# Kernel tuning notes

Measured on AMD Instinct MI355X. Metric: run time of the kernel, lower is better.

Reference implementation:

```python
import jax, jax.numpy as jnp
import numpy as np

B = 64        # graphs per batch
N = 1024      # nodes per graph
DEG = 16      # avg degree
E = B * N * DEG
F_IN = 10
H = 128
NC = 10
K1, K2, K3 = 205, 41, 9   # ceil(0.2 * prev_nodes_per_graph)


def _lin(key, fan_in, shape):
    return jax.random.normal(key, shape, jnp.float32) * (1.0 / np.sqrt(fan_in))


def setup_inputs() -> dict:
    key = jax.random.key(0)
    ks = jax.random.split(key, 32)
    x = jax.random.normal(ks[0], (B * N, F_IN), jnp.float32)
    # random intra-graph edges (source_to_target)
    src_l = jax.random.randint(ks[1], (B, N * DEG), 0, N)
    dst_l = jax.random.randint(ks[2], (B, N * DEG), 0, N)
    off = (jnp.arange(B) * N)[:, None]
    edge_index = jnp.stack([(src_l + off).reshape(-1), (dst_l + off).reshape(-1)]).astype(jnp.int32)
    inp = dict(x=x, edge_index=edge_index)
    inp["W1"] = _lin(ks[3], F_IN, (F_IN, H)); inp["b1"] = jnp.zeros((H,), jnp.float32)
    inp["W2"] = _lin(ks[4], H, (H, H));       inp["b2"] = jnp.zeros((H,), jnp.float32)
    inp["W3"] = _lin(ks[5], H, (H, H));       inp["b3"] = jnp.zeros((H,), jnp.float32)
    inp["Ws1"] = _lin(ks[6], H, (H, 1)); inp["bs1"] = jnp.zeros((1,), jnp.float32)
    inp["Ws2"] = _lin(ks[7], H, (H, 1)); inp["bs2"] = jnp.zeros((1,), jnp.float32)
    inp["Ws3"] = _lin(ks[8], H, (H, 1)); inp["bs3"] = jnp.zeros((1,), jnp.float32)
    inp["Wl1"] = _lin(ks[9], 2 * H, (2 * H, H));    inp["bl1"] = jnp.zeros((H,), jnp.float32)
    inp["Wl2"] = _lin(ks[10], H, (H, H // 2));      inp["bl2"] = jnp.zeros((H // 2,), jnp.float32)
    inp["Wl3"] = _lin(ks[11], H // 2, (H // 2, NC)); inp["bl3"] = jnp.zeros((NC,), jnp.float32)
    return inp


def gcn(x, W, b, src, dst, emask, n):
    """PyG GCNConv: symmetric norm with self-loops; masked edges contribute 0."""
    h = x @ W                                   # [n, out]
    w = emask.astype(h.dtype)                   # edge weights (0 for filtered edges)
    deg = jax.ops.segment_sum(w, dst, num_segments=n) + 1.0   # +1 self-loop
    dis = jax.lax.rsqrt(deg)                    # deg^{-1/2}
    norm = dis[src] * dis[dst] * w              # [E]
    out = jax.ops.segment_sum(h[src] * norm[:, None], dst, num_segments=n)
    out = out + h * (dis * dis)[:, None]        # self-loop message
    return out + b


def sagpool(x, src, dst, emask, Ws, bs, cur, k):
    """SAGPool: GCN score -> per-graph top-k -> gather + tanh gate -> filter_adj."""
    n = B * cur
    score = gcn(x, Ws, bs, src, dst, emask, n)[:, 0]          # [n]
    _, idx = jax.lax.top_k(score.reshape(B, cur), k)          # [B, k]
    perm = (idx + (jnp.arange(B) * cur)[:, None]).reshape(-1) # global node ids
    x = x[perm] * jnp.tanh(score[perm])[:, None]
    # filter_adj: remap node ids, drop edges with an unselected endpoint
    new_id = jnp.full((n,), -1, jnp.int32).at[perm].set(jnp.arange(B * k, dtype=jnp.int32))
    nsrc, ndst = new_id[src], new_id[dst]
    emask = emask & (nsrc >= 0) & (ndst >= 0)
    nsrc = jnp.where(emask, nsrc, 0)
    ndst = jnp.where(emask, ndst, 0)
    return x, nsrc, ndst, emask


def readout(x, k):
    xb = x.reshape(B, k, -1)
    return jnp.concatenate([xb.max(axis=1), xb.mean(axis=1)], axis=1)   # [B, 2H]


def reference(x, edge_index, W1, b1, W2, b2, W3, b3,
              Ws1, bs1, Ws2, bs2, Ws3, bs3,
              Wl1, bl1, Wl2, bl2, Wl3, bl3):
    src, dst = edge_index[0], edge_index[1]
    emask = jnp.ones((E,), bool)

    h = jax.nn.relu(gcn(x, W1, b1, src, dst, emask, B * N))
    h, src, dst, emask = sagpool(h, src, dst, emask, Ws1, bs1, N, K1)
    x1 = readout(h, K1)

    h = jax.nn.relu(gcn(h, W2, b2, src, dst, emask, B * K1))
    h, src, dst, emask = sagpool(h, src, dst, emask, Ws2, bs2, K1, K2)
    x2 = readout(h, K2)

    h = jax.nn.relu(gcn(h, W3, b3, src, dst, emask, B * K2))
    h, src, dst, emask = sagpool(h, src, dst, emask, Ws3, bs3, K2, K3)
    x3 = readout(h, K3)

    z = x1 + x2 + x3                             # [B, 2H]
    z = jax.nn.relu(z @ Wl1 + bl1)               # dropout is eval-mode identity
    z = jax.nn.relu(z @ Wl2 + bl2)
    return jax.nn.log_softmax(z @ Wl3 + bl3, axis=-1)
```

## Files before the change

### kernel.cpp

```cpp
#include <hip/hip_runtime.h>
#include <math.h>

#define NB 64
#define N0 1024
#define NEDGE 1048576
#define EPG 16384
#define FIN 10
#define NCLS 10
#define KP1 205
#define KP2 41
#define KP3 9

static inline int ceil_div(int a, int b) { return (a + b - 1) / b; }

__device__ __forceinline__ int block_scan_incl(int v, int* wtot, int lane, int wid) {
    __syncthreads();
    int x = v;
    #pragma unroll
    for (int s = 1; s < 64; s <<= 1) { int tv = __shfl_up(x, s); if (lane >= s) x += tv; }
    if (lane == 63) wtot[wid] = x;
    __syncthreads();
    if (wid == 0) {
        int w = (lane < 16) ? wtot[lane] : 0;
        #pragma unroll
        for (int s = 1; s < 16; s <<= 1) { int tv = __shfl_up(w, s); if (lane >= s) w += tv; }
        if (lane < 16) wtot[lane] = w;
    }
    __syncthreads();
    return x + ((wid > 0) ? wtot[wid - 1] : 0);
}

__device__ __forceinline__ unsigned fkey(float f) {
    unsigned b = __float_as_uint(f);
    return (f >= 0.f) ? (b | 0x80000000u) : ~b;
}

__global__ __launch_bounds__(1024) void build_csr1_k(const int* __restrict__ ei,
                                                     float* __restrict__ disg,
                                                     int* __restrict__ offg,
                                                     int* __restrict__ cntg,
                                                     int2* __restrict__ csr2) {
    __shared__ int cnt[N0];
    __shared__ int cur[N0];
    __shared__ float disl[N0];
    __shared__ int wtot[16];
    int b = blockIdx.x, t = threadIdx.x;
    int lane = t & 63, wid = t >> 6;
    cnt[t] = 0;
    __syncthreads();
    const int ebase = b * EPG;
    const int nbase = b * N0;
    #pragma unroll
    for (int u = 0; u < EPG / 1024; ++u) {
        int d = ei[NEDGE + ebase + u * 1024 + t] - nbase;
        atomicAdd(&cnt[d], 1);
    }
    __syncthreads();
    int v = cnt[t];
    int inc = block_scan_incl(v, wtot, lane, wid);
    int excl = inc - v;
    cur[t] = excl;
    float di = rsqrtf((float)v + 1.0f);
    disl[t] = di;
    offg[nbase + t] = ebase + excl;
    cntg[nbase + t] = v;
    disg[nbase + t] = di;
    __syncthreads();
    #pragma unroll
    for (int u = 0; u < EPG / 1024; ++u) {
        int j = ebase + u * 1024 + t;
        int s = ei[j], d = ei[NEDGE + j] - nbase;
        int pos = atomicAdd(&cur[d], 1);
        int2 o; o.x = s; o.y = __float_as_int(disl[s - nbase]);
        csr2[ebase + pos] = o;
    }
}

__global__ __launch_bounds__(256) void agg10_k(const float* __restrict__ x,
                                               const int2* __restrict__ csr2,
                                               const int* __restrict__ off,
                                               const int* __restrict__ cnt,
                                               const float* __restrict__ dis,
                                               float* __restrict__ y) {
    __shared__ float xl[N0 * 11];
    int b = blockIdx.x >> 2, chunk = blockIdx.x & 3;
    const float* xg = x + (size_t)b * (N0 * FIN);
    for (int u = threadIdx.x; u < N0 * FIN; u += 256) {
        int r = u / FIN, c = u - r * FIN;
        xl[r * 11 + c] = xg[u];
    }
    __syncthreads();
    int li = chunk * 256 + threadIdx.x;
    int i  = b * N0 + li;
    int s0 = off[i], m = cnt[i];
    int base = b * N0;
    float acc[FIN];
    #pragma unroll
    for (int f = 0; f < FIN; ++f) acc[f] = 0.f;
    int j = 0;
    for (; j + 2 <= m; j += 2) {
        int2 e0 = csr2[s0 + j], e1 = csr2[s0 + j + 1];
        int sl0 = (e0.x - base) * 11, sl1 = (e1.x - base) * 11;
        float w0 = __int_as_float(e0.y), w1 = __int_as_float(e1.y);
        #pragma unroll
        for (int f = 0; f < FIN; ++f) acc[f] += xl[sl0 + f] * w0 + xl[sl1 + f] * w1;
    }
    if (j < m) {
        int2 e0 = csr2[s0 + j];
        int sl0 = (e0.x - base) * 11;
        float w0 = __int_as_float(e0.y);
        #pragma unroll
        for (int f = 0; f < FIN; ++f) acc[f] += xl[sl0 + f] * w0;
    }
    float di = dis[i], d2 = di * di;
    #pragma unroll
    for (int f = 0; f < FIN; ++f)
        y[(size_t)i * FIN + f] = di * acc[f] + d2 * xl[li * 11 + f];
}

__global__ void gemm_fin_fused_k(const float* __restrict__ y, const float* __restrict__ W,
                                 const float* __restrict__ bb, const float* __restrict__ Wsc,
                                 const float* __restrict__ dis,
                                 float* __restrict__ hout, float* __restrict__ hs,
                                 float* __restrict__ hsd, int n) {
    __shared__ float Ws[FIN * 128];
    __shared__ float Sc[128];
    for (int u = threadIdx.x; u < FIN * 128; u += 256) Ws[u] = W[u];
    if (threadIdx.x < 128) Sc[threadIdx.x] = Wsc[threadIdx.x];
    __syncthreads();
    int t = blockIdx.x * 256 + threadIdx.x;
    int i = t >> 6, lane = threadIdx.x & 63;
    if (i >= n) return;
    float a = (lane < FIN) ? y[(size_t)i * FIN + lane] : 0.f;
    const float2* W2 = (const float2*)Ws;
    float ax = bb[lane * 2], ay = bb[lane * 2 + 1];
    #pragma unroll
    for (int k = 0; k < FIN; ++k) {
        float ak = __shfl(a, k);
        float2 w = W2[k * 64 + lane];
        ax += ak * w.x; ay += ak * w.y;
    }
    ax = fmaxf(ax, 0.f); ay = fmaxf(ay, 0.f);
    float2 o; o.x = ax; o.y = ay;
    ((float2*)hout)[(size_t)i * 64 + lane] = o;
    float part = ax * Sc[lane * 2] + ay * Sc[lane * 2 + 1];
    #pragma unroll
    for (int sh = 32; sh >= 1; sh >>= 1) part += __shfl_xor(part, sh);
    if (lane == 0) { hs[i] = part; hsd[i] = part * dis[i]; }
}

__global__ __launch_bounds__(1024) void s1_topk_build2_k(
    const float* __restrict__ hout, const float* __restrict__ hs,
    const float* __restrict__ hsd, const int* __restrict__ ei,
    int2* __restrict__ csr,
    const int* __restrict__ off1, const int* __restrict__ cnt1,
    const float* __restrict__ dis1, const float* __restrict__ bs1,
    float* __restrict__ hA, float* __restrict__ z, int* __restrict__ newid1,
    int* __restrict__ off2, int* __restrict__ cnt2g, float* __restrict__ dis2g,
    int* __restrict__ dst2, int* __restrict__ etot2) {
    __shared__ float hl[1024];
    __shared__ unsigned u[1024];
    __shared__ int wtot[16];
    __shared__ unsigned tinfo[2];
    __shared__ int   n1l[1024];
    __shared__ int   seln[KP1];
    __shared__ float gatel[KP1];
    __shared__ float zm[1024];
    __shared__ float zs[1024];
    __shared__ int   c2[KP1];
    __shared__ int   cur2[KP1];
    __shared__ float d2l[KP1];
    int b = blockIdx.x, t = threadIdx.x;
    int lane = t & 63, wid = t >> 6;
    const int nbase = b * N0, ebase = b * EPG;

    hl[t] = hsd[nbase + t];
    __syncthreads();
    float sc;
    {
        int s0 = off1[nbase + t], e0 = s0 + cnt1[nbase + t];
        float acc = 0.f;
        int j = s0;
        for (; j + 4 <= e0; j += 4) {
            int a0 = csr[j].x, a1 = csr[j+1].x, a2 = csr[j+2].x, a3 = csr[j+3].x;
            acc += hl[a0 - nbase] + hl[a1 - nbase] + hl[a2 - nbase] + hl[a3 - nbase];
        }
        for (; j < e0; ++j) acc += hl[csr[j].x - nbase];
        float di = dis1[nbase + t];
        sc = di * acc + hs[nbase + t] * (di * di) + bs1[0];
    }
    unsigned kb = fkey(sc);
    u[t] = kb;
    __syncthreads();
    if (wid == 0) {
        int remaining = KP1; unsigned prefix = 0;
        for (int bit = 31; bit >= 0; --bit) {
            int c = 0;
            #pragma unroll 4
            for (int i = lane; i < 1024; i += 64)
                c += ((u[i] >> bit) == ((prefix >> bit) | 1u));
            #pragma unroll
            for (int s = 32; s >= 1; s >>= 1) c += __shfl_xor(c, s);
            if (c >= remaining) prefix |= (1u << bit);
            else remaining -= c;
        }
        if (lane == 0) { tinfo[0] = prefix; tinfo[1] = (unsigned)remaining; }
    }
    __syncthreads();
    unsigned T = tinfo[0]; int extra = (int)tinfo[1];
    int gt = (kb > T), eq = (kb == T);
    int eqIncl = block_scan_incl(eq, wtot, lane, wid);
    int sel = gt || (eq && (eqIncl - eq) < extra);
    int selIncl = block_scan_incl(sel, wtot, lane, wid);
    int loc = selIncl - sel;
    if (sel) {
        n1l[t] = loc; seln[loc] = t; gatel[loc] = tanhf(sc);
        newid1[nbase + t] = b * KP1 + loc;
    } else {
        n1l[t] = -1; newid1[nbase + t] = -1;
    }
    __syncthreads();
    {
        int g = t >> 7, f = t & 127;
        float vmax = -INFINITY, vsum = 0.f;
        for (int j = g; j < KP1; j += 8) {
            int src = nbase + seln[j];
            float val = hout[(size_t)src * 128 + f] * gatel[j];
            hA[((size_t)b * KP1 + j) * 128 + f] = val;
            vmax = fmaxf(vmax, val); vsum += val;
        }
        zm[t] = vmax; zs[t] = vsum;
        __syncthreads();
        if (t < 128) {
            float m = zm[t], s2 = zs[t];
            #pragma unroll
            for (int g2 = 1; g2 < 8; ++g2) { m = fmaxf(m, zm[g2 * 128 + t]); s2 += zs[g2 * 128 + t]; }
            z[b * 256 + t] = m;
            z[b * 256 + 128 + t] = s2 / (float)KP1;
        }
    }
    __syncthreads();
    if (t < KP1) c2[t] = 0;
    __syncthreads();
    #pragma unroll
    for (int uu = 0; uu < EPG / 1024; ++uu) {
        int j = ebase + uu * 1024 + t;
        int s = ei[j] - nbase, d = ei[NEDGE + j] - nbase;
        int ls = n1l[s], ld = n1l[d];
        if (ls >= 0 && ld >= 0) atomicAdd(&c2[ld], 1);
    }
    __syncthreads();
    int vv = (t < KP1) ? c2[t] : 0;
    int inc = block_scan_incl(vv, wtot, lane, wid);
    int excl = inc - vv;
    if (t < KP1) {
        cur2[t] = excl;
        float dd = rsqrtf((float)vv + 1.0f);
        d2l[t] = dd;
        off2[b * KP1 + t] = ebase + excl;
        cnt2g[b * KP1 + t] = vv;
        dis2g[b * KP1 + t] = dd;
    }
    if (t == 1023) etot2[b] = inc;
    __syncthreads();
    #pragma unroll
    for (int uu = 0; uu < EPG / 1024; ++uu) {
        int j = ebase + uu * 1024 + t;
        int s = ei[j] - nbase, d = ei[NEDGE + j] - nbase;
        int ls = n1l[s], ld = n1l[d];
        if (ls < 0 || ld < 0) continue;
        int pos = atomicAdd(&cur2[ld], 1);
        int2 o; o.x = b * KP1 + ls; o.y = __float_as_int(d2l[ls]);
        csr[ebase + pos] = o;
        dst2[ebase + pos] = ld;
    }
}

__global__ __launch_bounds__(256) void gemm128_tiled_k(const float* __restrict__ A,
                                                       const float* __restrict__ W,
                                                       float* __restrict__ C, int n) {
    __shared__ float As[64][33];
    __shared__ float Wt[32][64];
    int tx = threadIdx.x & 15, ty = threadIdx.x >> 4;
    int r0 = blockIdx.x * 64;
    int c0 = blockIdx.y * 64;
    float4 acc0 = {0,0,0,0}, acc1 = {0,0,0,0}, acc2 = {0,0,0,0}, acc3 = {0,0,0,0};
    int u = threadIdx.x;
    for (int k0 = 0; k0 < 128; k0 += 32) {
        __syncthreads();
        {
            int rr = u >> 3, cc = (u & 7) * 4;
            #pragma unroll
            for (int h = 0; h < 2; ++h) {
                int r = rr + h * 32;
                float4 v = {0,0,0,0};
                if (r0 + r < n) v = *(const float4*)&A[(size_t)(r0 + r) * 128 + k0 + cc];
                As[r][cc] = v.x; As[r][cc+1] = v.y; As[r][cc+2] = v.z; As[r][cc+3] = v.w;
            }
        }
        {
            int kk = u >> 4, c = (u & 15) * 4;
            #pragma unroll
            for (int h = 0; h < 2; ++h) {
                float4 v = *(const float4*)&W[(size_t)(k0 + kk + h * 16) * 128 + c0 + c];
                *(float4*)&Wt[kk + h * 16][c] = v;
            }
        }
        __syncthreads();
        #pragma unroll
        for (int kk = 0; kk < 32; ++kk) {
            float4 wv = *(const float4*)&Wt[kk][tx * 4];
            float a0 = As[ty * 4 + 0][kk];
            float a1 = As[ty * 4 + 1][kk];
            float a2 = As[ty * 4 + 2][kk];
            float a3 = As[ty * 4 + 3][kk];
            acc0.x += a0 * wv.x; acc0.y += a0 * wv.y; acc0.z += a0 * wv.z; acc0.w += a0 * wv.w;
            acc1.x += a1 * wv.x; acc1.y += a1 * wv.y; acc1.z += a1 * wv.z; acc1.w += a1 * wv.w;
            acc2.x += a2 * wv.x; acc2.y += a2 * wv.y; acc2.z += a2 * wv.z; acc2.w += a2 * wv.w;
            acc3.x += a3 * wv.x; acc3.y += a3 * wv.y; acc3.z += a3 * wv.z; acc3.w += a3 * wv.w;
        }
    }
    int r = r0 + ty * 4;
    if (r + 0 < n) *(float4*)&C[(size_t)(r + 0) * 128 + c0 + tx * 4] = acc0;
    if (r + 1 < n) *(float4*)&C[(size_t)(r + 1) * 128 + c0 + tx * 4] = acc1;
    if (r + 2 < n) *(float4*)&C[(size_t)(r + 2) * 128 + c0 + tx * 4] = acc2;
    if (r + 3 < n) *(float4*)&C[(size_t)(r + 3) * 128 + c0 + tx * 4] = acc3;
}

__global__ void gcn_agg_fused2_k(const float* __restrict__ hW, const int2* __restrict__ csr2,
                                 const int* __restrict__ off, const int* __restrict__ cnt,
                                 const float* __restrict__ dis, const float* __restrict__ bias,
                                 const float* __restrict__ Wsc,
                                 float* __restrict__ hout, float* __restrict__ hs,
                                 float* __restrict__ hsd, int n, int cpx) {
    int wg = ((blockIdx.x & 7) * cpx) + (blockIdx.x >> 3);
    int t = wg * blockDim.x + threadIdx.x;
    int i = t >> 6;
    int lane = threadIdx.x & 63;
    if (i >= n) return;
    const float2* hW2 = (const float2*)hW;
    int s0 = off[i], e0 = s0 + cnt[i];
    float accx = 0.f, accy = 0.f;
    for (int j0 = s0; j0 < e0; j0 += 64) {
        int rem = e0 - j0;
        int m = rem < 64 ? rem : 64;
        int sv = 0; float wv = 0.f;
        if (lane < m) { int2 ec = csr2[j0 + lane]; sv = ec.x; wv = __int_as_float(ec.y); }
        int u = 0;
        for (; u + 4 <= m; u += 4) {
            int a0 = __shfl(sv, u + 0), a1 = __shfl(sv, u + 1);
            int a2 = __shfl(sv, u + 2), a3 = __shfl(sv, u + 3);
            float w0 = __shfl(wv, u + 0), w1 = __shfl(wv, u + 1);
            float w2 = __shfl(wv, u + 2), w3 = __shfl(wv, u + 3);
            float2 v0 = hW2[(size_t)a0 * 64 + lane];
            float2 v1 = hW2[(size_t)a1 * 64 + lane];
            float2 v2 = hW2[(size_t)a2 * 64 + lane];
            float2 v3 = hW2[(size_t)a3 * 64 + lane];
            accx += v0.x * w0 + v1.x * w1 + v2.x * w2 + v3.x * w3;
            accy += v0.y * w0 + v1.y * w1 + v2.y * w2 + v3.y * w3;
        }
        for (; u < m; ++u) {
            int s = __shfl(sv, u);
            float w = __shfl(wv, u);
            float2 v = hW2[(size_t)s * 64 + lane];
            accx += v.x * w; accy += v.y * w;
        }
    }
    float di = dis[i];
    float2 hv = hW2[(size_t)i * 64 + lane];
    float ox = fmaxf(di * accx + hv.x * (di * di) + bias[lane * 2], 0.f);
    float oy = fmaxf(di * accy + hv.y * (di * di) + bias[lane * 2 + 1], 0.f);
    float2 o; o.x = ox; o.y = oy;
    ((float2*)hout)[(size_t)i * 64 + lane] = o;
    float part = ox * Wsc[lane * 2] + oy * Wsc[lane * 2 + 1];
    #pragma unroll
    for (int sh = 32; sh >= 1; sh >>= 1) part += __shfl_xor(part, sh);
    if (lane == 0) { hs[i] = part; hsd[i] = part * di; }
}

__global__ __launch_bounds__(1024) void s2_topk_build3_k(
    const float* __restrict__ hout, const float* __restrict__ hs,
    const float* __restrict__ hsd,
    int2* __restrict__ csr, const int* __restrict__ dst2, const int* __restrict__ etot2,
    const int* __restrict__ off2, const int* __restrict__ cnt2,
    const float* __restrict__ dis2, const float* __restrict__ bs2,
    float* __restrict__ hA, float* __restrict__ z,
    int* __restrict__ off3, int* __restrict__ cnt3g, float* __restrict__ dis3g) {
    __shared__ float hl[256];
    __shared__ unsigned u2[256];
    __shared__ int wtot[16];
    __shared__ unsigned tinfo[2];
    __shared__ int   n2l[KP1];
    __shared__ int   seln[KP2];
    __shared__ float gatel[KP2];
    __shared__ float zm[1024];
    __shared__ float zs[1024];
    __shared__ int   c3[KP2];
    __shared__ int   cur3[KP2];
    __shared__ float d3l[KP2];
    int b = blockIdx.x, t = threadIdx.x;
    int lane = t & 63, wid = t >> 6;
    const int ebase = b * EPG;

    if (t < KP1) hl[t] = hsd[b * KP1 + t];
    __syncthreads();
    float sc = -INFINITY;
    if (t < KP1) {
        int i = b * KP1 + t;
        int s0 = off2[i], e0 = s0 + cnt2[i];
        float acc = 0.f;
        int j = s0;
        for (; j + 4 <= e0; j += 4) {
            int a0 = csr[j].x, a1 = csr[j+1].x, a2 = csr[j+2].x, a3 = csr[j+3].x;
            acc += hl[a0 - b*KP1] + hl[a1 - b*KP1] + hl[a2 - b*KP1] + hl[a3 - b*KP1];
        }
        for (; j < e0; ++j) acc += hl[csr[j].x - b*KP1];
        float di = dis2[i];
        sc = di * acc + hs[i] * (di * di) + bs2[0];
    }
    unsigned kb = fkey(sc);
    if (t < 256) u2[t] = kb;
    __syncthreads();
    if (wid == 0) {
        int remaining = KP2; unsigned prefix = 0;
        for (int bit = 31; bit >= 0; --bit) {
            int c = 0;
            #pragma unroll
            for (int i = lane; i < 256; i += 64)
                c += ((u2[i] >> bit) == ((prefix >> bit) | 1u));
            #pragma unroll
            for (int s = 32; s >= 1; s >>= 1) c += __shfl_xor(c, s);
            if (c >= remaining) prefix |= (1u << bit);
            else remaining -= c;
        }
        if (lane == 0) { tinfo[0] = prefix; tinfo[1] = (unsigned)remaining; }
    }
    __syncthreads();
    unsigned T = tinfo[0]; int extra = (int)tinfo[1];
    int valid = (t < KP1);
    int gt = valid && (kb > T), eq = valid && (kb == T);
    int eqIncl = block_scan_incl(eq, wtot, lane, wid);
    int sel = gt || (eq && (eqIncl - eq) < extra);
    int selIncl = block_scan_incl(sel, wtot, lane, wid);
    int loc = selIncl - sel;
    if (valid) {
        if (sel) { n2l[t] = loc; seln[loc] = t; gatel[loc] = tanhf(sc); }
        else     n2l[t] = -1;
    }
    __syncthreads();
    {
        int g = t >> 7, f = t & 127;
        float vmax = -INFINITY, vsum = 0.f;
        for (int j = g; j < KP2; j += 8) {
            int src = b * KP1 + seln[j];
            float val = hout[(size_t)src * 128 + f] * gatel[j];
            hA[((size_t)b * KP2 + j) * 128 + f] = val;
            vmax = fmaxf(vmax, val); vsum += val;
        }
        zm[t] = vmax; zs[t] = vsum;
        __syncthreads();
        if (t < 128) {
            float m = zm[t], s2 = zs[t];
            #pragma unroll
            for (int g2 = 1; g2 < 8; ++g2) { m = fmaxf(m, zm[g2 * 128 + t]); s2 += zs[g2 * 128 + t]; }
            z[b * 256 + t] += m;
            z[b * 256 + 128 + t] += s2 / (float)KP2;
        }
    }
    __syncthreads();
    int nE2 = etot2[b];
    int es[2], ed[2];
    #pragma unroll
    for (int r = 0; r < 2; ++r) {
        int i = r * 1024 + t;
        if (i < nE2) { es[r] = csr[ebase + i].x - b * KP1; ed[r] = dst2[ebase + i]; }
        else es[r] = -1;
    }
    __syncthreads();
    if (t < KP2) c3[t] = 0;
    __syncthreads();
    int ms[2], md[2];
    #pragma unroll
    for (int r = 0; r < 2; ++r) {
        ms[r] = -1;
        if (es[r] >= 0) {
            int ls = n2l[es[r]], ld = n2l[ed[r]];
            if (ls >= 0 && ld >= 0) { ms[r] = ls; md[r] = ld; atomicAdd(&c3[ld], 1); }
        }
    }
    __syncthreads();
    int vv = (t < KP2) ? c3[t] : 0;
    int inc = block_scan_incl(vv, wtot, lane, wid);
    int excl = inc - vv;
    if (t < KP2) {
        cur3[t] = excl;
        float dd = rsqrtf((float)vv + 1.0f);
        d3l[t] = dd;
        off3[b * KP2 + t] = ebase + excl;
        cnt3g[b * KP2 + t] = vv;
        dis3g[b * KP2 + t] = dd;
    }
    __syncthreads();
    #pragma unroll
    for (int r = 0; r < 2; ++r) {
        if (ms[r] < 0) continue;
        int pos = atomicAdd(&cur3[md[r]], 1);
        int2 o; o.x = b * KP2 + ms[r]; o.y = __float_as_int(d3l[ms[r]]);
        csr[ebase + pos] = o;
    }
}

__global__ __launch_bounds__(128) void s3_topk_mlp_k(
    const float* __restrict__ hout, const float* __restrict__ hs,
    const float* __restrict__ hsd, const int2* __restrict__ csr,
    const int* __restrict__ off3, const int* __restrict__ cnt3,
    const float* __restrict__ dis3, const float* __restrict__ bs3,
    const float* __restrict__ z,
    const float* __restrict__ Wl1, const float* __restrict__ bl1,
    const float* __restrict__ Wl2, const float* __restrict__ bl2,
    const float* __restrict__ Wl3, const float* __restrict__ bl3,
    float* __restrict__ out) {
    __shared__ float hl[KP2];
    __shared__ float v[64];
    __shared__ int   ix[64];
    __shared__ float zm[KP3];
    __shared__ float zr[256], h1[128], h2[64], lg[NCLS], red[2];
    int b = blockIdx.x, t = threadIdx.x;

    if (t < KP2) hl[t] = hsd[b * KP2 + t];
    __syncthreads();
    float sc = -INFINITY;
    if (t < KP2) {
        int i = b * KP2 + t;
        int s0 = off3[i], e0 = s0 + cnt3[i];
        float acc = 0.f;
        for (int j = s0; j < e0; ++j) acc += hl[csr[j].x - b*KP2];
        float di = dis3[i];
        sc = di * acc + hs[i] * (di * di) + bs3[0];
    }
    if (t < 64) { v[t] = sc; ix[t] = t; }
    __syncthreads();
    for (int size = 2; size <= 64; size <<= 1) {
        for (int stride = size >> 1; stride > 0; stride >>= 1) {
            if (t < 32) {
                int pos = 2 * t - (t & (stride - 1));
                int j2 = pos + stride;
                bool asc = (pos & size) == 0;
                float v0 = v[pos], v1 = v[j2];
                int i0 = ix[pos], i1 = ix[j2];
                bool jb = (v1 > v0) || (v1 == v0 && i1 < i0);
                bool sw = asc ? jb : !jb;
                if (sw) { v[pos] = v1; v[j2] = v0; ix[pos] = i1; ix[j2] = i0; }
            }
            __syncthreads();
        }
    }
    if (t < KP3) zm[t] = tanhf(v[t]);
    __syncthreads();
    {
        float vmax = -INFINITY, vsum = 0.f;
        #pragma unroll
        for (int j = 0; j < KP3; ++j) {
            int src = b * KP2 + ix[j];
            float val = hout[(size_t)src * 128 + t] * zm[j];
            vmax = fmaxf(vmax, val); vsum += val;
        }
        zr[t] = z[b * 256 + t] + vmax;
        zr[128 + t] = z[b * 256 + 128 + t] + vsum / (float)KP3;
    }
    __syncthreads();
    float acc = bl1[t];
    #pragma unroll 8
    for (int i = 0; i < 256; ++i) acc += zr[i] * Wl1[i * 128 + t];
    h1[t] = fmaxf(acc, 0.f);
    __syncthreads();
    if (t < 64) {
        float a2 = bl2[t];
        #pragma unroll 8
        for (int i = 0; i < 128; ++i) a2 += h1[i] * Wl2[i * 64 + t];
        h2[t] = fmaxf(a2, 0.f);
    }
    __syncthreads();
    if (t < NCLS) {
        float a3 = bl3[t];
        #pragma unroll 8
        for (int i = 0; i < 64; ++i) a3 += h2[i] * Wl3[i * NCLS + t];
        lg[t] = a3;
    }
    __syncthreads();
    if (t == 0) {
        float m = lg[0];
        for (int i = 1; i < NCLS; ++i) m = fmaxf(m, lg[i]);
        float s = 0.f;
        for (int i = 0; i < NCLS; ++i) s += expf(lg[i] - m);
        red[0] = m; red[1] = logf(s);
    }
    __syncthreads();
    if (t < NCLS) out[b * NCLS + t] = lg[t] - red[0] - red[1];
}

extern "C" void kernel_launch(void* const* d_in, const int* in_sizes, int n_in,
                              void* d_out, int out_size, void* d_ws, size_t ws_size,
                              hipStream_t stream) {
    const float* x   = (const float*)d_in[0];
    const int*   ei  = (const int*)d_in[1];
    const float* W1  = (const float*)d_in[2];  const float* b1  = (const float*)d_in[3];
    const float* W2  = (const float*)d_in[4];  const float* b2  = (const float*)d_in[5];
    const float* W3  = (const float*)d_in[6];  const float* b3  = (const float*)d_in[7];
    const float* Ws1 = (const float*)d_in[8];  const float* bs1 = (const float*)d_in[9];
    const float* Ws2 = (const float*)d_in[10]; const float* bs2 = (const float*)d_in[11];
    const float* Ws3 = (const float*)d_in[12]; const float* bs3 = (const float*)d_in[13];
    const float* Wl1 = (const float*)d_in[14]; const float* bl1 = (const float*)d_in[15];
    const float* Wl2 = (const float*)d_in[16]; const float* bl2 = (const float*)d_in[17];
    const float* Wl3 = (const float*)d_in[18]; const float* bl3 = (const float*)d_in[19];
    float* out = (float*)d_out;

    const int NMAX = NB * N0;
    const int N1 = NB * KP1;
    const int N2 = NB * KP2;

    char* p = (char*)d_ws;
    float* z      = (float*)p; p += (size_t)NB * 256 * 4;
    float* hW     = (float*)p; p += (size_t)N1 * 128 * 4;
    float* hout   = (float*)p; p += (size_t)NMAX * 128 * 4;
    float* hA     = (float*)p; p += (size_t)N1 * 128 * 4;
    float* y      = (float*)p; p += (size_t)NMAX * FIN * 4;
    float* dis1   = (float*)p; p += (size_t)NMAX * 4;
    float* hs     = (float*)p; p += (size_t)NMAX * 4;
    float* hsd    = (float*)p; p += (size_t)NMAX * 4;
    int* newid1   = (int*)p;   p += (size_t)NMAX * 4;
    int* off1     = (int*)p;   p += (size_t)NMAX * 4;
    int* cnt1     = (int*)p;   p += (size_t)NMAX * 4;
    int* off2     = (int*)p;   p += (size_t)N1 * 4;
    int* cnt2     = (int*)p;   p += (size_t)N1 * 4;
    float* dis2   = (float*)p; p += (size_t)N1 * 4;
    int* off3     = (int*)p;   p += (size_t)N2 * 4;
    int* cnt3     = (int*)p;   p += (size_t)N2 * 4;
    float* dis3   = (float*)p; p += (size_t)N2 * 4;
    int* dst2     = (int*)p;   p += (size_t)NEDGE * 4;
    int* etot2    = (int*)p;   p += (size_t)NB * 4;
    int2* csr2    = (int2*)p;  p += (size_t)NEDGE * 8;

    build_csr1_k<<<NB, 1024, 0, stream>>>(ei, dis1, off1, cnt1, csr2);
    agg10_k<<<NB * 4, 256, 0, stream>>>(x, csr2, off1, cnt1, dis1, y);
    gemm_fin_fused_k<<<NMAX / 4, 256, 0, stream>>>(y, W1, b1, Ws1, dis1, hout, hs, hsd, NMAX);
    s1_topk_build2_k<<<NB, 1024, 0, stream>>>(hout, hs, hsd, ei, csr2, off1, cnt1, dis1,
                                              bs1, hA, z, newid1, off2, cnt2, dis2,
                                              dst2, etot2);

    {
        dim3 g(ceil_div(N1, 64), 2);
        gemm128_tiled_k<<<g, 256, 0, stream>>>(hA, W2, hW, N1);
    }
    gcn_agg_fused2_k<<<N1 / 4, 256, 0, stream>>>(
        hW, csr2, off2, cnt2, dis2, b2, Ws2, hout, hs, hsd, N1, N1 / 32);
    s2_topk_build3_k<<<NB, 1024, 0, stream>>>(hout, hs, hsd, csr2, dst2, etot2,
                                              off2, cnt2, dis2, bs2, hA, z,
                                              off3, cnt3, dis3);

    {
        dim3 g(ceil_div(N2, 64), 2);
        gemm128_tiled_k<<<g, 256, 0, stream>>>(hA, W3, hW, N2);
    }
    gcn_agg_fused2_k<<<N2 / 4, 256, 0, stream>>>(
        hW, csr2, off3, cnt3, dis3, b3, Ws3, hout, hs, hsd, N2, N2 / 32);
    s3_topk_mlp_k<<<NB, 128, 0, stream>>>(hout, hs, hsd, csr2, off3, cnt3, dis3, bs3, z,
                                          Wl1, bl1, Wl2, bl2, Wl3, bl3, out);
}
```

Measured before the change: 271.2 us.

## Use radix-histogram top-k select, gather pooled rows in GEMM, cache edge registers

The top-k threshold search now runs as a 4-pass 8-bit radix histogram across the whole block, replacing the 32-pass bitwise search that used a single wavefront. Stage-1 pooling no longer writes the gated hA matrix. Instead it records selected row indices and gate values, and the next GEMM gathers rows from hout and applies the gate on load. Edge endpoints are kept in registers between the counting and scatter passes, so ei and the n1l lookups are not read twice. In exchange there are more block syncs per radix pass and an indirect row gather inside the GEMM load.

```diff
diff --git a/kernel.cpp b/kernel.cpp
--- a/kernel.cpp
+++ b/kernel.cpp
@@ -33,6 +33,39 @@
 __device__ __forceinline__ unsigned fkey(float f) {
     unsigned b = __float_as_uint(f);
     return (f >= 0.f) ? (b | 0x80000000u) : ~b;
+}
+
+__device__ __forceinline__ void hist_select_topk(const unsigned* keys, int nkeys, int K,
+                                                 int* hist, int* wtot, unsigned* tinfo,
+                                                 int t, int lane, int wid,
+                                                 unsigned& T, int& extra) {
+    unsigned prefix = 0; int remaining = K;
+    #pragma unroll
+    for (int r = 0; r < 4; ++r) {
+        int shift = 24 - 8 * r;
+        if (t < 256) hist[t] = 0;
+        __syncthreads();
+        unsigned himask = (r == 0) ? 0u : (0xFFFFFFFFu << (shift + 8));
+        for (int i = t; i < nkeys; i += 1024) {
+            unsigned k = keys[i];
+            if ((k & himask) == (prefix & himask))
+                atomicAdd(&hist[(k >> shift) & 255], 1);
+        }
+        __syncthreads();
+        int rv = (t < 256) ? hist[255 - t] : 0;
+        int inc = block_scan_incl(rv, wtot, lane, wid);
+        if (t < 256) {
+            int cntAbove = inc - rv;
+            if (cntAbove < remaining && inc >= remaining) {
+                tinfo[2] = (unsigned)(255 - t); tinfo[3] = (unsigned)cntAbove;
+            }
+        }
+        __syncthreads();
+        prefix |= (tinfo[2] << shift);
+        remaining -= (int)tinfo[3];
+        __syncthreads();
+    }
+    T = prefix; extra = remaining;
 }
 
 __global__ __launch_bounds__(1024) void build_csr1_k(const int* __restrict__ ei,
@@ -50,10 +83,13 @@
     __syncthreads();
     const int ebase = b * EPG;
     const int nbase = b * N0;
+    int sreg[EPG / 1024], dreg[EPG / 1024];
     #pragma unroll
     for (int u = 0; u < EPG / 1024; ++u) {
-        int d = ei[NEDGE + ebase + u * 1024 + t] - nbase;
-        atomicAdd(&cnt[d], 1);
+        int j = ebase + u * 1024 + t;
+        sreg[u] = ei[j] - nbase;
+        dreg[u] = ei[NEDGE + j] - nbase;
+        atomicAdd(&cnt[dreg[u]], 1);
     }
     __syncthreads();
     int v = cnt[t];
@@ -68,10 +104,8 @@
     __syncthreads();
     #pragma unroll
     for (int u = 0; u < EPG / 1024; ++u) {
-        int j = ebase + u * 1024 + t;
-        int s = ei[j], d = ei[NEDGE + j] - nbase;
-        int pos = atomicAdd(&cur[d], 1);
-        int2 o; o.x = s; o.y = __float_as_int(disl[s - nbase]);
+        int pos = atomicAdd(&cur[dreg[u]], 1);
+        int2 o; o.x = nbase + sreg[u]; o.y = __float_as_int(disl[sreg[u]]);
         csr2[ebase + pos] = o;
     }
 }
@@ -155,13 +189,14 @@
     int2* __restrict__ csr,
     const int* __restrict__ off1, const int* __restrict__ cnt1,
     const float* __restrict__ dis1, const float* __restrict__ bs1,
-    float* __restrict__ hA, float* __restrict__ z, int* __restrict__ newid1,
+    float* __restrict__ z, int* __restrict__ rows1, float* __restrict__ gate1,
     int* __restrict__ off2, int* __restrict__ cnt2g, float* __restrict__ dis2g,
     int* __restrict__ dst2, int* __restrict__ etot2) {
     __shared__ float hl[1024];
     __shared__ unsigned u[1024];
+    __shared__ int hist[256];
     __shared__ int wtot[16];
-    __shared__ unsigned tinfo[2];
+    __shared__ unsigned tinfo[4];
     __shared__ int   n1l[1024];
     __shared__ int   seln[KP1];
     __shared__ float gatel[KP1];
@@ -191,33 +226,20 @@
     }
     unsigned kb = fkey(sc);
     u[t] = kb;
-    __syncthreads();
-    if (wid == 0) {
-        int remaining = KP1; unsigned prefix = 0;
-        for (int bit = 31; bit >= 0; --bit) {
-            int c = 0;
-            #pragma unroll 4
-            for (int i = lane; i < 1024; i += 64)
-                c += ((u[i] >> bit) == ((prefix >> bit) | 1u));
-            #pragma unroll
-            for (int s = 32; s >= 1; s >>= 1) c += __shfl_xor(c, s);
-            if (c >= remaining) prefix |= (1u << bit);
-            else remaining -= c;
-        }
-        if (lane == 0) { tinfo[0] = prefix; tinfo[1] = (unsigned)remaining; }
-    }
-    __syncthreads();
-    unsigned T = tinfo[0]; int extra = (int)tinfo[1];
+    unsigned T; int extra;
+    hist_select_topk(u, 1024, KP1, hist, wtot, tinfo, t, lane, wid, T, extra);
     int gt = (kb > T), eq = (kb == T);
     int eqIncl = block_scan_incl(eq, wtot, lane, wid);
     int sel = gt || (eq && (eqIncl - eq) < extra);
     int selIncl = block_scan_incl(sel, wtot, lane, wid);
     int loc = selIncl - sel;
     if (sel) {
-        n1l[t] = loc; seln[loc] = t; gatel[loc] = tanhf(sc);
-        newid1[nbase + t] = b * KP1 + loc;
+        float g = tanhf(sc);
+        n1l[t] = loc; seln[loc] = t; gatel[loc] = g;
+        rows1[b * KP1 + loc] = nbase + t;
+        gate1[b * KP1 + loc] = g;
     } else {
-        n1l[t] = -1; newid1[nbase + t] = -1;
+        n1l[t] = -1;
     }
     __syncthreads();
     {
@@ -226,7 +248,6 @@
         for (int j = g; j < KP1; j += 8) {
             int src = nbase + seln[j];
             float val = hout[(size_t)src * 128 + f] * gatel[j];
-            hA[((size_t)b * KP1 + j) * 128 + f] = val;
             vmax = fmaxf(vmax, val); vsum += val;
         }
         zm[t] = vmax; zs[t] = vsum;
@@ -242,12 +263,14 @@
     __syncthreads();
     if (t < KP1) c2[t] = 0;
     __syncthreads();
+    int lsr[EPG / 1024], ldr[EPG / 1024];
     #pragma unroll
     for (int uu = 0; uu < EPG / 1024; ++uu) {
         int j = ebase + uu * 1024 + t;
         int s = ei[j] - nbase, d = ei[NEDGE + j] - nbase;
         int ls = n1l[s], ld = n1l[d];
-        if (ls >= 0 && ld >= 0) atomicAdd(&c2[ld], 1);
+        if (ls >= 0 && ld >= 0) { lsr[uu] = ls; ldr[uu] = ld; atomicAdd(&c2[ld], 1); }
+        else lsr[uu] = -1;
     }
     __syncthreads();
     int vv = (t < KP1) ? c2[t] : 0;
@@ -265,20 +288,19 @@
     __syncthreads();
     #pragma unroll
     for (int uu = 0; uu < EPG / 1024; ++uu) {
-        int j = ebase + uu * 1024 + t;
-        int s = ei[j] - nbase, d = ei[NEDGE + j] - nbase;
-        int ls = n1l[s], ld = n1l[d];
-        if (ls < 0 || ld < 0) continue;
-        int pos = atomicAdd(&cur2[ld], 1);
-        int2 o; o.x = b * KP1 + ls; o.y = __float_as_int(d2l[ls]);
+        if (lsr[uu] < 0) continue;
+        int pos = atomicAdd(&cur2[ldr[uu]], 1);
+        int2 o; o.x = b * KP1 + lsr[uu]; o.y = __float_as_int(d2l[lsr[uu]]);
         csr[ebase + pos] = o;
-        dst2[ebase + pos] = ld;
+        dst2[ebase + pos] = ldr[uu];
     }
 }
 
 __global__ __launch_bounds__(256) void gemm128_tiled_k(const float* __restrict__ A,
                                                        const float* __restrict__ W,
-                                                       float* __restrict__ C, int n) {
+                                                       float* __restrict__ C, int n,
+                                                       const int* __restrict__ rows,
+                                                       const float* __restrict__ gate) {
     __shared__ float As[64][33];
     __shared__ float Wt[32][64];
     int tx = threadIdx.x & 15, ty = threadIdx.x >> 4;
@@ -294,7 +316,14 @@
             for (int h = 0; h < 2; ++h) {
                 int r = rr + h * 32;
                 float4 v = {0,0,0,0};
-                if (r0 + r < n) v = *(const float4*)&A[(size_t)(r0 + r) * 128 + k0 + cc];
+                if (r0 + r < n) {
+                    int ar = rows ? rows[r0 + r] : (r0 + r);
+                    v = *(const float4*)&A[(size_t)ar * 128 + k0 + cc];
+                    if (gate) {
+                        float g = gate[r0 + r];
+                        v.x *= g; v.y *= g; v.z *= g; v.w *= g;
+                    }
+                }
                 As[r][cc] = v.x; As[r][cc+1] = v.y; As[r][cc+2] = v.z; As[r][cc+3] = v.w;
             }
         }
@@ -388,8 +417,9 @@
     int* __restrict__ off3, int* __restrict__ cnt3g, float* __restrict__ dis3g) {
     __shared__ float hl[256];
     __shared__ unsigned u2[256];
+    __shared__ int hist[256];
     __shared__ int wtot[16];
-    __shared__ unsigned tinfo[2];
+    __shared__ unsigned tinfo[4];
     __shared__ int   n2l[KP1];
     __shared__ int   seln[KP2];
     __shared__ float gatel[KP2];
@@ -418,25 +448,10 @@
         float di = dis2[i];
         sc = di * acc + hs[i] * (di * di) + bs2[0];
     }
-    unsigned kb = fkey(sc);
+    unsigned kb = (t < KP1) ? fkey(sc) : 0u;
     if (t < 256) u2[t] = kb;
-    __syncthreads();
-    if (wid == 0) {
-        int remaining = KP2; unsigned prefix = 0;
-        for (int bit = 31; bit >= 0; --bit) {
-            int c = 0;
-            #pragma unroll
-            for (int i = lane; i < 256; i += 64)
-                c += ((u2[i] >> bit) == ((prefix >> bit) | 1u));
-            #pragma unroll
-            for (int s = 32; s >= 1; s >>= 1) c += __shfl_xor(c, s);
-            if (c >= remaining) prefix |= (1u << bit);
-            else remaining -= c;
-        }
-        if (lane == 0) { tinfo[0] = prefix; tinfo[1] = (unsigned)remaining; }
-    }
-    __syncthreads();
-    unsigned T = tinfo[0]; int extra = (int)tinfo[1];
+    unsigned T; int extra;
+    hist_select_topk(u2, 256, KP2, hist, wtot, tinfo, t, lane, wid, T, extra);
     int valid = (t < KP1);
     int gt = valid && (kb > T), eq = valid && (kb == T);
     int eqIncl = block_scan_incl(eq, wtot, lane, wid);
@@ -628,9 +643,10 @@
     float* dis1   = (float*)p; p += (size_t)NMAX * 4;
     float* hs     = (float*)p; p += (size_t)NMAX * 4;
     float* hsd    = (float*)p; p += (size_t)NMAX * 4;
-    int* newid1   = (int*)p;   p += (size_t)NMAX * 4;
     int* off1     = (int*)p;   p += (size_t)NMAX * 4;
     int* cnt1     = (int*)p;   p += (size_t)NMAX * 4;
+    int* rows1    = (int*)p;   p += (size_t)N1 * 4;
+    float* gate1  = (float*)p; p += (size_t)N1 * 4;
     int* off2     = (int*)p;   p += (size_t)N1 * 4;
     int* cnt2     = (int*)p;   p += (size_t)N1 * 4;
     float* dis2   = (float*)p; p += (size_t)N1 * 4;
@@ -645,12 +661,12 @@
     agg10_k<<<NB * 4, 256, 0, stream>>>(x, csr2, off1, cnt1, dis1, y);
     gemm_fin_fused_k<<<NMAX / 4, 256, 0, stream>>>(y, W1, b1, Ws1, dis1, hout, hs, hsd, NMAX);
     s1_topk_build2_k<<<NB, 1024, 0, stream>>>(hout, hs, hsd, ei, csr2, off1, cnt1, dis1,
-                                              bs1, hA, z, newid1, off2, cnt2, dis2,
+                                              bs1, z, rows1, gate1, off2, cnt2, dis2,
                                               dst2, etot2);
 
     {
         dim3 g(ceil_div(N1, 64), 2);
-        gemm128_tiled_k<<<g, 256, 0, stream>>>(hA, W2, hW, N1);
+        gemm128_tiled_k<<<g, 256, 0, stream>>>(hout, W2, hW, N1, rows1, gate1);
     }
     gcn_agg_fused2_k<<<N1 / 4, 256, 0, stream>>>(
         hW, csr2, off2, cnt2, dis2, b2, Ws2, hout, hs, hsd, N1, N1 / 32);
@@ -660,7 +676,7 @@
 
     {
         dim3 g(ceil_div(N2, 64), 2);
-        gemm128_tiled_k<<<g, 256, 0, stream>>>(hA, W3, hW, N2);
+        gemm128_tiled_k<<<g, 256, 0, stream>>>(hA, W3, hW, N2, nullptr, nullptr);
     }
     gcn_agg_fused2_k<<<N2 / 4, 256, 0, stream>>>(
         hW, csr2, off3, cnt3, dis3, b3, Ws3, hout, hs, hsd, N2, N2 / 32);
```

Measured after the change: 252.8 us. 1.07x faster.
